# Kernel tuning notes

Measured on AMD Instinct MI355X. Metric: run time of the kernel, lower is better.

The kernel has to match this reference:

```python
import jax, jax.numpy as jnp
import numpy as np

B, C, H, W = 8, 64, 64, 64
DQK = C // 8  # q/k projection dim = 8


def setup_inputs() -> dict:
    key = jax.random.key(0)
    ks = jax.random.split(key, 5)
    return {
        "query": jax.random.normal(ks[0], (B, C, H, W), dtype=jnp.float32),
        "value": jax.random.normal(ks[1], (B, C, H, W), dtype=jnp.float32),
        "Wq": jax.random.normal(ks[2], (DQK, C), dtype=jnp.float32) * (1.0 / np.sqrt(C)),
        "bq": jnp.zeros((DQK,), dtype=jnp.float32),
        "Wk": jax.random.normal(ks[3], (DQK, C), dtype=jnp.float32) * (1.0 / np.sqrt(C)),
        "bk": jnp.zeros((DQK,), dtype=jnp.float32),
        "Wv": jax.random.normal(ks[4], (C, C), dtype=jnp.float32) * (1.0 / np.sqrt(C)),
        "bv": jnp.zeros((C,), dtype=jnp.float32),
    }


def reference(query, value, Wq, bq, Wk, bk, Wv, bv):
    b, c, h, w = value.shape
    n = h * w
    # 1x1 convs are per-pixel matmuls over channels
    q = jnp.einsum("oc,bchw->bohw", Wq, query) + bq[None, :, None, None]
    k = jnp.einsum("oc,bchw->bohw", Wk, query) + bk[None, :, None, None]
    v = jnp.einsum("oc,bchw->bohw", Wv, value) + bv[None, :, None, None]
    proj_q = q.reshape(b, DQK, n).transpose(0, 2, 1)  # [B, N, d]
    proj_k = k.reshape(b, DQK, n)                      # [B, d, N]
    energy = jnp.einsum("bnd,bdm->bnm", proj_q, proj_k)  # [B, N, N]
    attention = jax.nn.softmax(energy, axis=-1)
    proj_v = v.reshape(b, c, n)                        # [B, C, N]
    # out = proj_v @ attention^T
    out = jnp.einsum("bcm,bnm->bcn", proj_v, attention)
    out = out.reshape(b, c, h, w) + value
    return out
```

## Files before the change

### kernel.cpp

```cpp
#include <hip/hip_runtime.h>
#include <hip/hip_bf16.h>

typedef __attribute__((ext_vector_type(8))) __bf16 bf16x8;
typedef __attribute__((ext_vector_type(4))) float f32x4;

#if __has_builtin(__builtin_amdgcn_exp2f)
#define EXP2F(x) __builtin_amdgcn_exp2f(x)
#else
#define EXP2F(x) exp2f(x)
#endif

static constexpr int BB = 8, CC = 64, NN = 4096;
static constexpr size_t QF_OFF = 0;
static constexpr size_t KF_OFF = (size_t)2 << 20;
static constexpr size_t VF_OFF = (size_t)4 << 20;


__global__ __launch_bounds__(256) void proj_kernel(
    const float* __restrict__ query, const float* __restrict__ value,
    const float* __restrict__ Wq, const float* __restrict__ bq,
    const float* __restrict__ Wk, const float* __restrict__ bk,
    const float* __restrict__ Wv, const float* __restrict__ bv,
    char* __restrict__ ws) {
  __shared__ __bf16 vlds[64][68];
  __shared__ float  qlds[64][9];
  __shared__ float  klds[64][9];
  const float LOG2E = 1.4426950408889634f;
  int t = threadIdx.x;
  int part = __builtin_amdgcn_readfirstlane(t >> 6);
  int px = t & 63;
  int blk = blockIdx.x;
  int b = blk >> 6;
  int px0 = (blk & 63) << 6;
  size_t inbase = (size_t)b * CC * NN + px0 + px;

  int qko = (part >> 1) << 2;
  bool isq = (part & 1) == 0;
  const float* __restrict__ Wqk = isq ? Wq : Wk;

  float xq[64];
  #pragma unroll
  for (int c = 0; c < 64; ++c) xq[c] = query[inbase + (size_t)c * NN];
  float qk[4] = {0.f, 0.f, 0.f, 0.f};
  #pragma unroll
  for (int c = 0; c < 64; ++c) {
    #pragma unroll
    for (int o = 0; o < 4; ++o) qk[o] += Wqk[(qko + o) * 64 + c] * xq[c];
  }
  if (isq) {
    #pragma unroll
    for (int o = 0; o < 4; ++o) qlds[px][qko + o] = (qk[o] + bq[qko + o]) * LOG2E;
  } else {
    #pragma unroll
    for (int o = 0; o < 4; ++o) klds[px][qko + o] = qk[o] + bk[qko + o];
  }

  float xv[64];
  #pragma unroll
  for (int c = 0; c < 64; ++c) xv[c] = value[inbase + (size_t)c * NN];
  float vacc[16];
  #pragma unroll
  for (int o = 0; o < 16; ++o) vacc[o] = bv[part * 16 + o];
  #pragma unroll
  for (int c = 0; c < 64; ++c) {
    #pragma unroll
    for (int o = 0; o < 16; ++o) vacc[o] += Wv[(part * 16 + o) * 64 + c] * xv[c];
  }
  #pragma unroll
  for (int o = 0; o < 16; ++o) vlds[px][part * 16 + o] = (__bf16)vacc[o];
  __syncthreads();

  __bf16* qfrag = (__bf16*)(ws + QF_OFF);
  __bf16* kfrag = (__bf16*)(ws + KF_OFF);
  __bf16* vfrag = (__bf16*)(ws + VF_OFF);
  int l = t & 63, cp = l & 15, qd = l >> 4;
  int ct = t >> 6;

  #pragma unroll
  for (int jt = 0; jt < 2; ++jt) {
    bf16x8 v8;
    #pragma unroll
    for (int r = 0; r < 8; ++r) {
      int jj = (r < 4) ? (4 * qd + r) : (16 + 4 * qd + (r & 3));
      v8[r] = vlds[jt * 32 + jj][ct * 16 + cp];
    }
    int jtg = (blk & 63) * 2 + jt;
    *(bf16x8*)(vfrag + ((((size_t)b * 128 + jtg) * 4 + ct) * 64 + l) * 8) = v8;
  }
  {
    int jt = t >> 7, th = (t >> 6) & 1;
    int pxl = jt * 32 + th * 16 + (l & 15);
    bf16x8 k8;
    #pragma unroll
    for (int r = 0; r < 8; ++r) {
      float kv = klds[pxl][r];
      __bf16 hi = (__bf16)kv;
      __bf16 lo = (__bf16)(kv - (float)hi);
      k8[r] = (qd < 2) ? hi : (qd == 2 ? lo : (__bf16)0.f);
    }
    int jtg = (blk & 63) * 2 + jt;
    *(bf16x8*)(kfrag + ((((size_t)b * 128 + jtg) * 2 + th) * 64 + l) * 8) = k8;
  }
  {
    int il = ct * 16 + (l & 15);
    bf16x8 q8;
    #pragma unroll
    for (int r = 0; r < 8; ++r) {
      float qv = qlds[il][r];
      __bf16 hi = (__bf16)qv;
      __bf16 lo = (__bf16)(qv - (float)hi);
      q8[r] = (qd == 0 || qd == 2) ? hi : (qd == 1 ? lo : (__bf16)0.f);
    }
    int itg = (blk & 63) * 4 + ct;
    *(bf16x8*)(qfrag + (((size_t)b * 256 + itg) * 64 + l) * 8) = q8;
  }
}

__global__ __launch_bounds__(256, 2) void attn_kernel(
    const char* __restrict__ ws, const float* __restrict__ value,
    float* __restrict__ out) {
  __shared__ float lds_acc[32 * 4 * 64];
  __shared__ float lds_l[16 * 64];
  const __bf16* qfrag = (const __bf16*)(ws + QF_OFF);
  const __bf16* kfrag = (const __bf16*)(ws + KF_OFF);
  const __bf16* vfrag = (const __bf16*)(ws + VF_OFF);
  int tid = threadIdx.x;
  int w = tid >> 6, lane = tid & 63;
  int blk = blockIdx.x;
  int b = blk >> 6;
  int i0 = (blk & 63) << 6;
  int itg0 = (blk & 63) * 4;

  bf16x8 qf[4];
  #pragma unroll
  for (int it = 0; it < 4; ++it)
    qf[it] = *(const bf16x8*)(qfrag + (((size_t)b * 256 + itg0 + it) * 64 + lane) * 8);

  f32x4 acc[4][4];
  #pragma unroll
  for (int ct = 0; ct < 4; ++ct)
    #pragma unroll
    for (int it = 0; it < 4; ++it) acc[ct][it] = (f32x4){0.f, 0.f, 0.f, 0.f};
  float lsum[4] = {0.f, 0.f, 0.f, 0.f};

  const __bf16* kb = kfrag + (((size_t)b * 128 + w * 32) * 2 * 64 + lane) * 8;
  const __bf16* vb = vfrag + (((size_t)b * 128 + w * 32) * 4 * 64 + lane) * 8;

  for (int itx = 0; itx < 32; ++itx) {
    bf16x8 kf0 = *(const bf16x8*)(kb);
    bf16x8 kf1 = *(const bf16x8*)(kb + 512);
    bf16x8 vf0 = *(const bf16x8*)(vb);
    bf16x8 vf1 = *(const bf16x8*)(vb + 512);
    bf16x8 vf2 = *(const bf16x8*)(vb + 1024);
    bf16x8 vf3 = *(const bf16x8*)(vb + 1536);
    const f32x4 z = (f32x4){0.f, 0.f, 0.f, 0.f};
    bf16x8 pf[4];
    #pragma unroll
    for (int it = 0; it < 4; ++it) {
      f32x4 e0 = __builtin_amdgcn_mfma_f32_16x16x32_bf16(kf0, qf[it], z, 0, 0, 0);
      f32x4 e1 = __builtin_amdgcn_mfma_f32_16x16x32_bf16(kf1, qf[it], z, 0, 0, 0);
      #pragma unroll
      for (int g = 0; g < 4; ++g) {
        float p0 = EXP2F(e0[g]); lsum[it] += p0; pf[it][g] = (__bf16)p0;
        float p1 = EXP2F(e1[g]); lsum[it] += p1; pf[it][4 + g] = (__bf16)p1;
      }
    }
    #pragma unroll
    for (int it = 0; it < 4; ++it) {
      acc[0][it] = __builtin_amdgcn_mfma_f32_16x16x32_bf16(vf0, pf[it], acc[0][it], 0, 0, 0);
      acc[1][it] = __builtin_amdgcn_mfma_f32_16x16x32_bf16(vf1, pf[it], acc[1][it], 0, 0, 0);
      acc[2][it] = __builtin_amdgcn_mfma_f32_16x16x32_bf16(vf2, pf[it], acc[2][it], 0, 0, 0);
      acc[3][it] = __builtin_amdgcn_mfma_f32_16x16x32_bf16(vf3, pf[it], acc[3][it], 0, 0, 0);
    }
    kb += 1024;
    vb += 2048;
  }

  #pragma unroll
  for (int it = 0; it < 4; ++it) {
    lsum[it] += __shfl_xor(lsum[it], 16, 64);
    lsum[it] += __shfl_xor(lsum[it], 32, 64);
    lds_l[(it * 4 + w) * 64 + lane] = lsum[it];
  }

  int ect = tid >> 6, l = tid & 63;
  #pragma unroll
  for (int p = 0; p < 2; ++p) {
    if (p) __syncthreads();
    #pragma unroll
    for (int ct = 0; ct < 4; ++ct)
      #pragma unroll
      for (int itl = 0; itl < 2; ++itl)
        #pragma unroll
        for (int r = 0; r < 4; ++r) {
          int e = ct * 8 + itl * 4 + r;
          lds_acc[(e * 4 + w) * 64 + lane] = acc[ct][2 * p + itl][r];
        }
    __syncthreads();
    #pragma unroll
    for (int itl = 0; itl < 2; ++itl) {
      int it = 2 * p + itl;
      float ls = 0.f;
      #pragma unroll
      for (int ww = 0; ww < 4; ++ww) ls += lds_l[(it * 4 + ww) * 64 + (l & 15)];
      float inv = 1.0f / ls;
      int n = i0 + it * 16 + (l & 15);
      #pragma unroll
      for (int r = 0; r < 4; ++r) {
        int e = ect * 8 + itl * 4 + r;
        float s = 0.f;
        #pragma unroll
        for (int ww = 0; ww < 4; ++ww) s += lds_acc[(e * 4 + ww) * 64 + l];
        int c = ect * 16 + (l >> 4) * 4 + r;
        size_t idx = ((size_t)b * CC + c) * NN + n;
        out[idx] = s * inv + value[idx];
      }
    }
  }
}

extern "C" void kernel_launch(void* const* d_in, const int* in_sizes, int n_in,
                              void* d_out, int out_size, void* d_ws, size_t ws_size,
                              hipStream_t stream) {
  const float* query = (const float*)d_in[0];
  const float* value = (const float*)d_in[1];
  const float* Wq = (const float*)d_in[2];
  const float* bq = (const float*)d_in[3];
  const float* Wk = (const float*)d_in[4];
  const float* bk = (const float*)d_in[5];
  const float* Wv = (const float*)d_in[6];
  const float* bv = (const float*)d_in[7];
  float* out = (float*)d_out;

  proj_kernel<<<512, 256, 0, stream>>>(query, value, Wq, bq, Wk, bk, Wv, bv, (char*)d_ws);
  attn_kernel<<<512, 256, 0, stream>>>((const char*)d_ws, value, out);
}
```

Before: 124.7 us.

## Double block size to 512 threads, split key range across eight waves

Both kernels now launch 512 threads per block. In the attention kernel each of eight waves handles 16 key tiles instead of 32, and the cross-wave reduction is widened to eight partials. The probability fragment is consumed right after the exp, which lowers register pressure and allows a four-blocks-per-CU launch bound. The projection kernel splits the output channels across eight parts and interleaves the query and value loads in chunks of 16 channels. The aim is more waves in flight to hide latency, paid for with extra LDS reduction work and more synchronisation.

```diff
diff --git a/kernel.cpp b/kernel.cpp
--- a/kernel.cpp
+++ b/kernel.cpp
@@ -16,13 +16,13 @@
 static constexpr size_t VF_OFF = (size_t)4 << 20;
 
 
-__global__ __launch_bounds__(256) void proj_kernel(
+__global__ __launch_bounds__(512) void proj_kernel(
     const float* __restrict__ query, const float* __restrict__ value,
     const float* __restrict__ Wq, const float* __restrict__ bq,
     const float* __restrict__ Wk, const float* __restrict__ bk,
     const float* __restrict__ Wv, const float* __restrict__ bv,
     char* __restrict__ ws) {
-  __shared__ __bf16 vlds[64][68];
+  __shared__ __bf16 vlds[64][72];
   __shared__ float  qlds[64][9];
   __shared__ float  klds[64][9];
   const float LOG2E = 1.4426950408889634f;
@@ -34,50 +34,52 @@
   int px0 = (blk & 63) << 6;
   size_t inbase = (size_t)b * CC * NN + px0 + px;
 
-  int qko = (part >> 1) << 2;
-  bool isq = (part & 1) == 0;
+  bool isq = part < 4;
+  int qko = (part & 3) * 2;
   const float* __restrict__ Wqk = isq ? Wq : Wk;
 
-  float xq[64];
-  #pragma unroll
-  for (int c = 0; c < 64; ++c) xq[c] = query[inbase + (size_t)c * NN];
-  float qk[4] = {0.f, 0.f, 0.f, 0.f};
-  #pragma unroll
-  for (int c = 0; c < 64; ++c) {
-    #pragma unroll
-    for (int o = 0; o < 4; ++o) qk[o] += Wqk[(qko + o) * 64 + c] * xq[c];
-  }
+  float vacc[8];
+  #pragma unroll
+  for (int o = 0; o < 8; ++o) vacc[o] = bv[part * 8 + o];
+  float qk0 = 0.f, qk1 = 0.f;
+
+  #pragma unroll
+  for (int cb = 0; cb < 4; ++cb) {
+    float xq[16], xv[16];
+    #pragma unroll
+    for (int cc = 0; cc < 16; ++cc) {
+      int c = cb * 16 + cc;
+      xq[cc] = query[inbase + (size_t)c * NN];
+      xv[cc] = value[inbase + (size_t)c * NN];
+    }
+    #pragma unroll
+    for (int cc = 0; cc < 16; ++cc) {
+      int c = cb * 16 + cc;
+      qk0 += Wqk[qko * 64 + c] * xq[cc];
+      qk1 += Wqk[(qko + 1) * 64 + c] * xq[cc];
+      #pragma unroll
+      for (int o = 0; o < 8; ++o) vacc[o] += Wv[(part * 8 + o) * 64 + c] * xv[cc];
+    }
+  }
+
+  #pragma unroll
+  for (int o = 0; o < 8; ++o) vlds[px][part * 8 + o] = (__bf16)vacc[o];
   if (isq) {
-    #pragma unroll
-    for (int o = 0; o < 4; ++o) qlds[px][qko + o] = (qk[o] + bq[qko + o]) * LOG2E;
+    qlds[px][qko]     = (qk0 + bq[qko]) * LOG2E;
+    qlds[px][qko + 1] = (qk1 + bq[qko + 1]) * LOG2E;
   } else {
-    #pragma unroll
-    for (int o = 0; o < 4; ++o) klds[px][qko + o] = qk[o] + bk[qko + o];
-  }
-
-  float xv[64];
-  #pragma unroll
-  for (int c = 0; c < 64; ++c) xv[c] = value[inbase + (size_t)c * NN];
-  float vacc[16];
-  #pragma unroll
-  for (int o = 0; o < 16; ++o) vacc[o] = bv[part * 16 + o];
-  #pragma unroll
-  for (int c = 0; c < 64; ++c) {
-    #pragma unroll
-    for (int o = 0; o < 16; ++o) vacc[o] += Wv[(part * 16 + o) * 64 + c] * xv[c];
-  }
-  #pragma unroll
-  for (int o = 0; o < 16; ++o) vlds[px][part * 16 + o] = (__bf16)vacc[o];
+    klds[px][qko]     = qk0 + bk[qko];
+    klds[px][qko + 1] = qk1 + bk[qko + 1];
+  }
   __syncthreads();
 
   __bf16* qfrag = (__bf16*)(ws + QF_OFF);
   __bf16* kfrag = (__bf16*)(ws + KF_OFF);
   __bf16* vfrag = (__bf16*)(ws + VF_OFF);
   int l = t & 63, cp = l & 15, qd = l >> 4;
-  int ct = t >> 6;
-
-  #pragma unroll
-  for (int jt = 0; jt < 2; ++jt) {
+
+  {
+    int jt = t >> 8, ct = (t >> 6) & 3;
     bf16x8 v8;
     #pragma unroll
     for (int r = 0; r < 8; ++r) {
@@ -87,7 +89,7 @@
     int jtg = (blk & 63) * 2 + jt;
     *(bf16x8*)(vfrag + ((((size_t)b * 128 + jtg) * 4 + ct) * 64 + l) * 8) = v8;
   }
-  {
+  if (t < 256) {
     int jt = t >> 7, th = (t >> 6) & 1;
     int pxl = jt * 32 + th * 16 + (l & 15);
     bf16x8 k8;
@@ -96,31 +98,31 @@
       float kv = klds[pxl][r];
       __bf16 hi = (__bf16)kv;
       __bf16 lo = (__bf16)(kv - (float)hi);
-      k8[r] = (qd < 2) ? hi : (qd == 2 ? lo : (__bf16)0.f);
+      k8[r] = (qd < 2) ? hi : lo;
     }
     int jtg = (blk & 63) * 2 + jt;
     *(bf16x8*)(kfrag + ((((size_t)b * 128 + jtg) * 2 + th) * 64 + l) * 8) = k8;
-  }
-  {
-    int il = ct * 16 + (l & 15);
+  } else {
+    int it = (t >> 6) & 3;
+    int il = it * 16 + (l & 15);
     bf16x8 q8;
     #pragma unroll
     for (int r = 0; r < 8; ++r) {
       float qv = qlds[il][r];
       __bf16 hi = (__bf16)qv;
       __bf16 lo = (__bf16)(qv - (float)hi);
-      q8[r] = (qd == 0 || qd == 2) ? hi : (qd == 1 ? lo : (__bf16)0.f);
-    }
-    int itg = (blk & 63) * 4 + ct;
+      q8[r] = ((qd & 1) == 0) ? hi : lo;
+    }
+    int itg = (blk & 63) * 4 + it;
     *(bf16x8*)(qfrag + (((size_t)b * 256 + itg) * 64 + l) * 8) = q8;
   }
 }
 
-__global__ __launch_bounds__(256, 2) void attn_kernel(
+__global__ __launch_bounds__(512, 4) void attn_kernel(
     const char* __restrict__ ws, const float* __restrict__ value,
     float* __restrict__ out) {
-  __shared__ float lds_acc[32 * 4 * 64];
-  __shared__ float lds_l[16 * 64];
+  __shared__ float lds_acc[16 * 8 * 64];
+  __shared__ float lds_l[4 * 8 * 64];
   const __bf16* qfrag = (const __bf16*)(ws + QF_OFF);
   const __bf16* kfrag = (const __bf16*)(ws + KF_OFF);
   const __bf16* vfrag = (const __bf16*)(ws + VF_OFF);
@@ -143,10 +145,10 @@
     for (int it = 0; it < 4; ++it) acc[ct][it] = (f32x4){0.f, 0.f, 0.f, 0.f};
   float lsum[4] = {0.f, 0.f, 0.f, 0.f};
 
-  const __bf16* kb = kfrag + (((size_t)b * 128 + w * 32) * 2 * 64 + lane) * 8;
-  const __bf16* vb = vfrag + (((size_t)b * 128 + w * 32) * 4 * 64 + lane) * 8;
-
-  for (int itx = 0; itx < 32; ++itx) {
+  const __bf16* kb = kfrag + (((size_t)b * 128 + w * 16) * 2 * 64 + lane) * 8;
+  const __bf16* vb = vfrag + (((size_t)b * 128 + w * 16) * 4 * 64 + lane) * 8;
+
+  for (int itx = 0; itx < 16; ++itx) {
     bf16x8 kf0 = *(const bf16x8*)(kb);
     bf16x8 kf1 = *(const bf16x8*)(kb + 512);
     bf16x8 vf0 = *(const bf16x8*)(vb);
@@ -154,23 +156,20 @@
     bf16x8 vf2 = *(const bf16x8*)(vb + 1024);
     bf16x8 vf3 = *(const bf16x8*)(vb + 1536);
     const f32x4 z = (f32x4){0.f, 0.f, 0.f, 0.f};
-    bf16x8 pf[4];
     #pragma unroll
     for (int it = 0; it < 4; ++it) {
       f32x4 e0 = __builtin_amdgcn_mfma_f32_16x16x32_bf16(kf0, qf[it], z, 0, 0, 0);
       f32x4 e1 = __builtin_amdgcn_mfma_f32_16x16x32_bf16(kf1, qf[it], z, 0, 0, 0);
+      bf16x8 pf;
       #pragma unroll
       for (int g = 0; g < 4; ++g) {
-        float p0 = EXP2F(e0[g]); lsum[it] += p0; pf[it][g] = (__bf16)p0;
-        float p1 = EXP2F(e1[g]); lsum[it] += p1; pf[it][4 + g] = (__bf16)p1;
+        float p0 = EXP2F(e0[g]); lsum[it] += p0; pf[g] = (__bf16)p0;
+        float p1 = EXP2F(e1[g]); lsum[it] += p1; pf[4 + g] = (__bf16)p1;
       }
-    }
-    #pragma unroll
-    for (int it = 0; it < 4; ++it) {
-      acc[0][it] = __builtin_amdgcn_mfma_f32_16x16x32_bf16(vf0, pf[it], acc[0][it], 0, 0, 0);
-      acc[1][it] = __builtin_amdgcn_mfma_f32_16x16x32_bf16(vf1, pf[it], acc[1][it], 0, 0, 0);
-      acc[2][it] = __builtin_amdgcn_mfma_f32_16x16x32_bf16(vf2, pf[it], acc[2][it], 0, 0, 0);
-      acc[3][it] = __builtin_amdgcn_mfma_f32_16x16x32_bf16(vf3, pf[it], acc[3][it], 0, 0, 0);
+      acc[0][it] = __builtin_amdgcn_mfma_f32_16x16x32_bf16(vf0, pf, acc[0][it], 0, 0, 0);
+      acc[1][it] = __builtin_amdgcn_mfma_f32_16x16x32_bf16(vf1, pf, acc[1][it], 0, 0, 0);
+      acc[2][it] = __builtin_amdgcn_mfma_f32_16x16x32_bf16(vf2, pf, acc[2][it], 0, 0, 0);
+      acc[3][it] = __builtin_amdgcn_mfma_f32_16x16x32_bf16(vf3, pf, acc[3][it], 0, 0, 0);
     }
     kb += 1024;
     vb += 2048;
@@ -180,41 +179,33 @@
   for (int it = 0; it < 4; ++it) {
     lsum[it] += __shfl_xor(lsum[it], 16, 64);
     lsum[it] += __shfl_xor(lsum[it], 32, 64);
-    lds_l[(it * 4 + w) * 64 + lane] = lsum[it];
-  }
-
-  int ect = tid >> 6, l = tid & 63;
-  #pragma unroll
-  for (int p = 0; p < 2; ++p) {
+    lds_l[(it * 8 + w) * 64 + lane] = lsum[it];
+  }
+
+  int l = tid & 63;
+  #pragma unroll
+  for (int p = 0; p < 4; ++p) {
     if (p) __syncthreads();
     #pragma unroll
     for (int ct = 0; ct < 4; ++ct)
       #pragma unroll
-      for (int itl = 0; itl < 2; ++itl)
-        #pragma unroll
-        for (int r = 0; r < 4; ++r) {
-          int e = ct * 8 + itl * 4 + r;
-          lds_acc[(e * 4 + w) * 64 + lane] = acc[ct][2 * p + itl][r];
-        }
+      for (int r = 0; r < 4; ++r)
+        lds_acc[((ct * 4 + r) * 8 + w) * 64 + lane] = acc[ct][p][r];
     __syncthreads();
-    #pragma unroll
-    for (int itl = 0; itl < 2; ++itl) {
-      int it = 2 * p + itl;
-      float ls = 0.f;
-      #pragma unroll
-      for (int ww = 0; ww < 4; ++ww) ls += lds_l[(it * 4 + ww) * 64 + (l & 15)];
-      float inv = 1.0f / ls;
-      int n = i0 + it * 16 + (l & 15);
-      #pragma unroll
-      for (int r = 0; r < 4; ++r) {
-        int e = ect * 8 + itl * 4 + r;
-        float s = 0.f;
-        #pragma unroll
-        for (int ww = 0; ww < 4; ++ww) s += lds_acc[(e * 4 + ww) * 64 + l];
-        int c = ect * 16 + (l >> 4) * 4 + r;
-        size_t idx = ((size_t)b * CC + c) * NN + n;
-        out[idx] = s * inv + value[idx];
-      }
+    float ls = 0.f;
+    #pragma unroll
+    for (int ww = 0; ww < 8; ++ww) ls += lds_l[(p * 8 + ww) * 64 + (l & 15)];
+    float inv = 1.0f / ls;
+    int n = i0 + p * 16 + (l & 15);
+    #pragma unroll
+    for (int r2 = 0; r2 < 2; ++r2) {
+      int e = (tid >> 6) * 2 + r2;
+      float s = 0.f;
+      #pragma unroll
+      for (int ww = 0; ww < 8; ++ww) s += lds_acc[(e * 8 + ww) * 64 + l];
+      int c = (e >> 2) * 16 + (l >> 4) * 4 + (e & 3);
+      size_t idx = ((size_t)b * CC + c) * NN + n;
+      out[idx] = s * inv + value[idx];
     }
   }
 }
@@ -232,6 +223,6 @@
   const float* bv = (const float*)d_in[7];
   float* out = (float*)d_out;
 
-  proj_kernel<<<512, 256, 0, stream>>>(query, value, Wq, bq, Wk, bk, Wv, bv, (char*)d_ws);
-  attn_kernel<<<512, 256, 0, stream>>>((const char*)d_ws, value, out);
+  proj_kernel<<<512, 512, 0, stream>>>(query, value, Wq, bq, Wk, bk, Wv, bv, (char*)d_ws);
+  attn_kernel<<<512, 512, 0, stream>>>((const char*)d_ws, value, out);
 }
```

Result: no change. 126.8 us (+1.7%).
